# Kernel optimization log

Hardware: AMD Instinct MI355X
Metric: run time of the kernel (lower is better)

Reference implementation:

```python
import jax, jax.numpy as jnp
import numpy as np

B, NQ, NP, C, H = 8, 1024, 2048, 1024, 16
D = C // H  # head_dim = 64


def setup_inputs() -> dict:
    key = jax.random.key(0)
    ks = jax.random.split(key, 12)
    s = 1.0 / np.sqrt(C)
    inp = {
        "x": jax.random.normal(ks[0], (B, NQ, C), dtype=jnp.float32),
        "ctx": jax.random.normal(ks[1], (B, NP, C), dtype=jnp.float32),
        "freqs_cis": jax.random.normal(ks[2], (NP, D // 2, 2), dtype=jnp.float32),
        "wq": jax.random.normal(ks[3], (C, C), dtype=jnp.float32) * s,
        "bq": jnp.zeros((C,), dtype=jnp.float32),
        "wk": jax.random.normal(ks[4], (C, C), dtype=jnp.float32) * s,
        "bk": jnp.zeros((C,), dtype=jnp.float32),
        "wv": jax.random.normal(ks[5], (C, C), dtype=jnp.float32) * s,
        "bv": jnp.zeros((C,), dtype=jnp.float32),
        "wo": jax.random.normal(ks[6], (C, C), dtype=jnp.float32) * s,
        "bo": jnp.zeros((C,), dtype=jnp.float32),
    }
    return inp


def _apply_rope(k, freqs_cis):
    # k: [B, Np, H, D]; freqs_cis: [Np, D//2, 2] (cos, sin)
    b, n, h, d = k.shape
    kp = k.reshape(b, n, h, d // 2, 2)  # adjacent-pair complex convention
    kr, ki = kp[..., 0], kp[..., 1]
    cos = freqs_cis[None, :, None, :, 0]
    sin = freqs_cis[None, :, None, :, 1]
    out_r = kr * cos - ki * sin
    out_i = kr * sin + ki * cos
    return jnp.stack([out_r, out_i], axis=-1).reshape(b, n, h, d)


def reference(x, ctx, freqs_cis, wq, bq, wk, bk, wv, bv, wo, bo):
    b, nq, c = x.shape
    npx = ctx.shape[1]
    q = (jnp.einsum('bsc,oc->bso', x, wq) + bq).reshape(b, nq, H, D)
    k = (jnp.einsum('bsc,oc->bso', ctx, wk) + bk).reshape(b, npx, H, D)
    v = (jnp.einsum('bsc,oc->bso', ctx, wv) + bv).reshape(b, npx, H, D)
    k = _apply_rope(k, freqs_cis)
    scale = 1.0 / jnp.sqrt(jnp.asarray(D, dtype=q.dtype))
    scores = jnp.einsum('bqhd,bkhd->bhqk', q, k) * scale
    attn = jax.nn.softmax(scores, axis=-1)
    out = jnp.einsum('bhqk,bkhd->bqhd', attn, v).reshape(b, nq, c)
    return jnp.einsum('bsc,oc->bso', out, wo) + bo
```

## Files before the change

### kernel.cpp

```cpp
#include <hip/hip_runtime.h>
#include <stdint.h>

typedef __bf16 bf16;
typedef bf16 bf16x8 __attribute__((ext_vector_type(8)));
typedef float f32x4 __attribute__((ext_vector_type(4)));
typedef float f32x16 __attribute__((ext_vector_type(16)));
typedef uint32_t u32x4 __attribute__((ext_vector_type(4)));

static __device__ __forceinline__ void async_cp16(const bf16* gsrc, bf16* ldst) {
  __builtin_amdgcn_global_load_lds(
      (const __attribute__((address_space(1))) uint32_t*)gsrc,
      (__attribute__((address_space(3))) uint32_t*)ldst, 16, 0, 0);
}

static __device__ __forceinline__ f32x16 mfma32(bf16x8 a, bf16x8 b, f32x16 c) {
  return __builtin_amdgcn_mfma_f32_32x32x16_bf16(a, b, c, 0, 0, 0);
}
static __device__ __forceinline__ f32x4 mfma16(bf16x8 a, bf16x8 b, f32x4 c) {
  return __builtin_amdgcn_mfma_f32_16x16x32_bf16(a, b, c, 0, 0, 0);
}

static __device__ __forceinline__ uint32_t cvtpk(float lo, float hi) {
  uint32_t r;
  asm("v_cvt_pk_bf16_f32 %0, %1, %2" : "=v"(r) : "v"(lo), "v"(hi));
  return r;
}
static __device__ __forceinline__ void plswap(uint32_t& a, uint32_t& b) {
  asm("v_permlane32_swap_b32 %0, %1" : "+v"(a), "+v"(b));
}

__global__ __launch_bounds__(256) void convert_all(
    const float* __restrict__ x, const float* __restrict__ ctx,
    const float* __restrict__ wq, const float* __restrict__ wk,
    const float* __restrict__ wv, const float* __restrict__ wo,
    bf16* __restrict__ xb, bf16* __restrict__ cb,
    bf16* __restrict__ wqb, bf16* __restrict__ wkb,
    bf16* __restrict__ wvb, bf16* __restrict__ wob) {
  int id = blockIdx.x;
  const float* s; bf16* d; int base;
  if (id < 8192)        { s = x;   d = xb;  base = id; }
  else if (id < 24576)  { s = ctx; d = cb;  base = id - 8192; }
  else if (id < 25600)  { s = wq;  d = wqb; base = id - 24576; }
  else if (id < 26624)  { s = wk;  d = wkb; base = id - 25600; }
  else if (id < 27648)  { s = wv;  d = wvb; base = id - 26624; }
  else                  { s = wo;  d = wob; base = id - 27648; }
  int i = base * 256 + threadIdx.x;
  float4 v = ((const float4*)s)[i];
  ushort4 o;
  o.x = __builtin_bit_cast(unsigned short, (bf16)v.x);
  o.y = __builtin_bit_cast(unsigned short, (bf16)v.y);
  o.z = __builtin_bit_cast(unsigned short, (bf16)v.z);
  o.w = __builtin_bit_cast(unsigned short, (bf16)v.w);
  ((ushort4*)d)[i] = o;
}

template <int OUT_F32, int BIAS_ROW = 0, int ROPE = 0>
__global__ __launch_bounds__(256) void gemm_bt(
    const bf16* __restrict__ A, const bf16* __restrict__ Bw,
    const float* __restrict__ bias, void* __restrict__ Cout,
    int M, int N, int K, float oscale, const float* __restrict__ freqs) {
  __shared__ __align__(16) bf16 sA[128 * 32];
  __shared__ __align__(16) bf16 sB[128 * 32];

  int per = gridDim.x >> 3;
  int id = blockIdx.x;
  int swz = (id & 7) * per + (id >> 3);
  int NB = N >> 7;
  int mb = swz / NB, nb = swz % NB;

  int t = threadIdx.x;
  int l = t & 63, w = t >> 6;
  int wr = (w >> 1) * 64, wc = (w & 1) * 64;
  int lr = l & 15, lk = (l >> 4) * 8;

  const bf16* Abase = A + (size_t)(mb * 128 + (t >> 2)) * K + (t & 3) * 8;
  const bf16* Bbase = Bw + (size_t)(nb * 128 + (t >> 2)) * K + (t & 3) * 8;
  bf16* ldsA = sA + w * 512;
  bf16* ldsB = sB + w * 512;

  f32x4 acc[4][4];
  for (int i = 0; i < 4; i++)
    for (int j = 0; j < 4; j++) acc[i][j] = f32x4{0.f, 0.f, 0.f, 0.f};

  for (int k0 = 0; k0 < K; k0 += 32) {
    async_cp16(Abase + k0, ldsA);
    async_cp16(Abase + k0 + (size_t)64 * K, ldsA + 2048);
    async_cp16(Bbase + k0, ldsB);
    async_cp16(Bbase + k0 + (size_t)64 * K, ldsB + 2048);
    __syncthreads();
    bf16x8 af[4], bfr[4];
    for (int mf = 0; mf < 4; mf++)
      af[mf] = *(const bf16x8*)&sA[(wr + mf * 16 + lr) * 32 + lk];
    for (int nf = 0; nf < 4; nf++)
      bfr[nf] = *(const bf16x8*)&sB[(wc + nf * 16 + lr) * 32 + lk];
    for (int mf = 0; mf < 4; mf++)
      for (int nf = 0; nf < 4; nf++)
        acc[mf][nf] = mfma16(af[mf], bfr[nf], acc[mf][nf]);
    __syncthreads();
  }

  int row0 = mb * 128 + wr + (l >> 4) * 4;
  int col0 = nb * 128 + wc + lr;
  float sgn = (lr & 1) ? 1.f : -1.f;
  for (int nf = 0; nf < 4; nf++) {
    int c = col0 + nf * 16;
    float bi = BIAS_ROW ? 0.f : bias[c];
    for (int mf = 0; mf < 4; mf++)
      for (int j = 0; j < 4; j++) {
        int r = row0 + mf * 16 + j;
        float v = acc[mf][nf][j] + (BIAS_ROW ? bias[r] : bi);
        if (ROPE) {
          float pv = __shfl_xor(v, 1, 64);
          float2 f = ((const float2*)freqs)[(size_t)(r & 2047) * 32 + ((c & 63) >> 1)];
          v = v * f.x + sgn * pv * f.y;
        }
        v *= oscale;
        if (OUT_F32)
          ((float*)Cout)[(size_t)r * N + c] = v;
        else
          ((bf16*)Cout)[(size_t)r * N + c] = (bf16)v;
      }
  }
}

template <int OUT_F32, int BIAS_ROW, int ROPE>
__global__ __launch_bounds__(512, 2) void gemm256(
    const bf16* __restrict__ A, const bf16* __restrict__ Bw,
    const float* __restrict__ bias, void* __restrict__ Cout,
    int N, int K, float oscale, const float* __restrict__ freqs) {
  __shared__ __align__(16) bf16 sA[2][16384];
  __shared__ __align__(16) bf16 sB[2][16384];

  int per = gridDim.x >> 3;
  int id = blockIdx.x;
  int swz = (id & 7) * per + (id >> 3);
  int NB = N >> 8;
  int mb = swz / NB, nb = swz % NB;

  int tid = threadIdx.x;
  int l = tid & 63, w = tid >> 6;
  int wm = w >> 2, wn = w & 3;
  int lr = l & 15, kg = l >> 4;

  int rw = w * 8 + (l >> 3);
  int cs = ((l & 7) ^ ((l >> 3) & 7)) * 8;
  const bf16* Ab = A + (size_t)(mb * 256 + rw) * K + cs;
  const bf16* Bb = Bw + (size_t)(nb * 256 + rw) * K + cs;

  auto stA = [&](int kt, int half, int buf) {
    const bf16* g = Ab + (size_t)(half * 128) * K + kt * 64;
    bf16* d = &sA[buf][half * 8192 + w * 512];
    async_cp16(g, d);
    async_cp16(g + (size_t)64 * K, d + 4096);
  };
  auto stB = [&](int kt, int half, int buf) {
    const bf16* g = Bb + (size_t)(half * 128) * K + kt * 64;
    bf16* d = &sB[buf][half * 8192 + w * 512];
    async_cp16(g, d);
    async_cp16(g + (size_t)64 * K, d + 4096);
  };

  f32x4 acc[8][4];
#pragma unroll
  for (int i = 0; i < 8; i++)
#pragma unroll
    for (int j = 0; j < 4; j++) acc[i][j] = f32x4{0.f, 0.f, 0.f, 0.f};

  int NT = K >> 6;

  stA(0, 0, 0); stA(0, 1, 0); stB(0, 0, 0); stB(0, 1, 0);
  asm volatile("s_waitcnt vmcnt(0)" ::: "memory");
  __builtin_amdgcn_s_barrier();

  int cur = 0;
  for (int t = 0; t < NT; ++t) {
    bool pf = (t + 1 < NT);
    if (pf) {
      stA(t + 1, 0, cur ^ 1);
      asm volatile("s_waitcnt vmcnt(2)" ::: "memory");
    } else {
      asm volatile("s_waitcnt vmcnt(0)" ::: "memory");
    }
    __builtin_amdgcn_s_barrier();

    const bf16* pA = sA[cur];
    const bf16* pB = sB[cur];
    bf16x8 afr[4][2], bq0[2][2], bq1[2][2];

    auto rdA = [&](int mh, int mf, int ks) {
      int rT = wm * 128 + mh * 64 + mf * 16 + lr;
      return *(const bf16x8*)&pA[rT * 64 + (((ks << 2) | kg) ^ (lr & 7)) * 8];
    };
    auto rdB = [&](int nfg, int ks) {
      int rT = wn * 64 + nfg * 16 + lr;
      return *(const bf16x8*)&pB[rT * 64 + (((ks << 2) | kg) ^ (lr & 7)) * 8];
    };

#pragma unroll
    for (int mf = 0; mf < 4; mf++) { afr[mf][0] = rdA(0, mf, 0); afr[mf][1] = rdA(0, mf, 1); }
#pragma unroll
    for (int nf = 0; nf < 2; nf++) { bq0[nf][0] = rdB(nf, 0); bq0[nf][1] = rdB(nf, 1); }
    __builtin_amdgcn_s_barrier();
    __builtin_amdgcn_s_setprio(1);
#pragma unroll
    for (int mf = 0; mf < 4; mf++)
#pragma unroll
      for (int nf = 0; nf < 2; nf++)
#pragma unroll
        for (int ks = 0; ks < 2; ks++)
          acc[mf][nf] = mfma16(afr[mf][ks], bq0[nf][ks], acc[mf][nf]);
    __builtin_amdgcn_s_setprio(0);
    __builtin_amdgcn_s_barrier();

#pragma unroll
    for (int nf = 0; nf < 2; nf++) { bq1[nf][0] = rdB(2 + nf, 0); bq1[nf][1] = rdB(2 + nf, 1); }
    if (pf) stA(t + 1, 1, cur ^ 1);
    __builtin_amdgcn_s_barrier();
    __builtin_amdgcn_s_setprio(1);
#pragma unroll
    for (int mf = 0; mf < 4; mf++)
#pragma unroll
      for (int nf = 0; nf < 2; nf++)
#pragma unroll
        for (int ks = 0; ks < 2; ks++)
          acc[mf][2 + nf] = mfma16(afr[mf][ks], bq1[nf][ks], acc[mf][2 + nf]);
    __builtin_amdgcn_s_setprio(0);
    __builtin_amdgcn_s_barrier();

#pragma unroll
    for (int mf = 0; mf < 4; mf++) { afr[mf][0] = rdA(1, mf, 0); afr[mf][1] = rdA(1, mf, 1); }
    if (pf) stB(t + 1, 0, cur ^ 1);
    __builtin_amdgcn_s_barrier();
    __builtin_amdgcn_s_setprio(1);
#pragma unroll
    for (int mf = 0; mf < 4; mf++)
#pragma unroll
      for (int nf = 0; nf < 2; nf++)
#pragma unroll
        for (int ks = 0; ks < 2; ks++)
          acc[4 + mf][2 + nf] = mfma16(afr[mf][ks], bq1[nf][ks], acc[4 + mf][2 + nf]);
    __builtin_amdgcn_s_setprio(0);
    __builtin_amdgcn_s_barrier();

    if (pf) stB(t + 1, 1, cur ^ 1);
    __builtin_amdgcn_s_barrier();
    __builtin_amdgcn_s_setprio(1);
#pragma unroll
    for (int mf = 0; mf < 4; mf++)
#pragma unroll
      for (int nf = 0; nf < 2; nf++)
#pragma unroll
        for (int ks = 0; ks < 2; ks++)
          acc[4 + mf][nf] = mfma16(afr[mf][ks], bq0[nf][ks], acc[4 + mf][nf]);
    __builtin_amdgcn_s_setprio(0);
    __builtin_amdgcn_s_barrier();

    cur ^= 1;
  }

  int row0 = mb * 256 + wm * 128 + (l >> 4) * 4;
  int col0 = nb * 256 + wn * 64 + lr;
  float sgn = (lr & 1) ? 1.f : -1.f;
#pragma unroll
  for (int fc = 0; fc < 4; fc++) {
    int c = col0 + fc * 16;
    float bi = BIAS_ROW ? 0.f : bias[c];
#pragma unroll
    for (int fr = 0; fr < 8; fr++) {
#pragma unroll
      for (int j = 0; j < 4; j++) {
        int r = row0 + fr * 16 + j;
        float v = acc[fr][fc][j] + (BIAS_ROW ? bias[r] : bi);
        if (ROPE) {
          float pv = __shfl_xor(v, 1, 64);
          float2 f = ((const float2*)freqs)[(size_t)(r & 2047) * 32 + ((c & 63) >> 1)];
          v = v * f.x + sgn * pv * f.y;
        }
        v *= oscale;
        if (OUT_F32)
          ((float*)Cout)[(size_t)r * N + c] = v;
        else
          ((bf16*)Cout)[(size_t)r * N + c] = (bf16)v;
      }
    }
  }
}

__global__ __launch_bounds__(256, 4) void attn_fwd(
    const bf16* __restrict__ Q, const bf16* __restrict__ Kb,
    const bf16* __restrict__ VT, bf16* __restrict__ O) {
  __shared__ __align__(16) bf16 sK[2][4096];
  __shared__ __align__(16) bf16 sV[2][4096];

  int nblk = blockIdx.x;
  int bh = (nblk & 7) * 16 + (nblk >> 6);
  int qt = (nblk >> 3) & 7;
  int b = bh >> 4, h = bh & 15;

  int t = threadIdx.x, l = t & 63, w = t >> 6;
  int ln = l & 31, hi = l >> 5;

  int qg = qt * 128 + w * 32 + ln;
  const bf16* qp = Q + ((size_t)(b * 1024 + qg) * 16 + h) * 64 + hi * 8;
  bf16x8 qf[4];
#pragma unroll
  for (int ds = 0; ds < 4; ds++) qf[ds] = *(const bf16x8*)(qp + ds * 16);

  const bf16* kbase = Kb + ((size_t)b * 2048 * 16 + h) * 64;
  const bf16* vtbase = VT + (size_t)(h * 64) * 16384 + b * 2048;

  int krow = w * 8 + (l >> 3);
  int cg1 = ((l & 7) ^ (krow & 7) ^ ((krow >> 3) & 7)) * 8;
  int r2 = krow + 32;
  int cg2 = ((l & 7) ^ (r2 & 7) ^ ((r2 >> 3) & 7)) * 8;

  auto stageK = [&](int kv0, int nb) {
    async_cp16(kbase + (size_t)(kv0 + krow) * 1024 + cg1, &sK[nb][w * 512]);
    async_cp16(kbase + (size_t)(kv0 + r2) * 1024 + cg2, &sK[nb][2048 + w * 512]);
  };
  auto stageV = [&](int kv0, int nb) {
    async_cp16(vtbase + (size_t)krow * 16384 + kv0 + cg1, &sV[nb][w * 512]);
    async_cp16(vtbase + (size_t)r2 * 16384 + kv0 + cg2, &sV[nb][2048 + w * 512]);
  };

  f32x16 o0, o1, s0, s1, lacc, zero16;
#pragma unroll
  for (int i = 0; i < 16; i++) {
    o0[i] = 0.f; o1[i] = 0.f; lacc[i] = 0.f; zero16[i] = 0.f;
  }
  uint32_t one2 = 0x3f803f80u;
  u32x4 onesw; onesw[0] = one2; onesw[1] = one2; onesw[2] = one2; onesw[3] = one2;
  bf16x8 onesf = __builtin_bit_cast(bf16x8, onesw);

  stageK(0, 0);
  stageV(0, 0);
  __syncthreads();
  int cur = 0;

  int x0 = ((ln & 7) ^ (ln >> 3)) << 3;
  int x1 = x0 ^ (4 << 3);

  for (int tt = 0; tt < 32; tt++) {
    if (tt < 31) { stageK(tt * 64 + 64, cur ^ 1); stageV(tt * 64 + 64, cur ^ 1); }

    __builtin_amdgcn_s_setprio(1);
    {
      int boff = hi * 8;
      bf16x8 kf0 = *(const bf16x8*)&sK[cur][ln * 64 + (boff ^ x0)];
      bf16x8 kf1 = *(const bf16x8*)&sK[cur][(ln + 32) * 64 + (boff ^ x1)];
      s0 = mfma32(kf0, qf[0], zero16);
      s1 = mfma32(kf1, qf[0], zero16);
    }
#pragma unroll
    for (int ds = 1; ds < 4; ds++) {
      int boff = ds * 16 + hi * 8;
      bf16x8 kf0 = *(const bf16x8*)&sK[cur][ln * 64 + (boff ^ x0)];
      bf16x8 kf1 = *(const bf16x8*)&sK[cur][(ln + 32) * 64 + (boff ^ x1)];
      s0 = mfma32(kf0, qf[ds], s0);
      s1 = mfma32(kf1, qf[ds], s1);
    }
    __builtin_amdgcn_s_setprio(0);

#pragma unroll
    for (int i = 0; i < 16; i++) {
      s0[i] = __builtin_amdgcn_exp2f(s0[i]);
      s1[i] = __builtin_amdgcn_exp2f(s1[i]);
    }

    bf16x8 pa[4];
    auto mkfrags = [&](const f32x16& sv, int base) {
#pragma unroll
      for (int u = 0; u < 2; u++) {
        uint32_t w0a = cvtpk(sv[8 * u + 0], sv[8 * u + 1]);
        uint32_t w0b = cvtpk(sv[8 * u + 4], sv[8 * u + 5]);
        plswap(w0a, w0b);
        uint32_t w1a = cvtpk(sv[8 * u + 2], sv[8 * u + 3]);
        uint32_t w1b = cvtpk(sv[8 * u + 6], sv[8 * u + 7]);
        plswap(w1a, w1b);
        u32x4 tmp;
        tmp[0] = w0a; tmp[1] = w1a; tmp[2] = w0b; tmp[3] = w1b;
        pa[base + u] = __builtin_bit_cast(bf16x8, tmp);
      }
    };
    mkfrags(s0, 0);
    mkfrags(s1, 2);

    __builtin_amdgcn_s_setprio(1);
#pragma unroll
    for (int ks = 0; ks < 4; ks++) {
      int koff = ks * 16 + hi * 8;
      bf16x8 vf0 = *(const bf16x8*)&sV[cur][ln * 64 + (koff ^ x0)];
      bf16x8 vf1 = *(const bf16x8*)&sV[cur][(ln + 32) * 64 + (koff ^ x1)];
      o0 = mfma32(vf0, pa[ks], o0);
      o1 = mfma32(vf1, pa[ks], o1);
      lacc = mfma32(onesf, pa[ks], lacc);
    }
    __builtin_amdgcn_s_setprio(0);

    __syncthreads();
    cur ^= 1;
  }

  float inv = __builtin_amdgcn_rcpf(lacc[0]);
  bf16* obase = O + ((size_t)(b * 1024 + qt * 128 + w * 32 + ln) * 16 + h) * 64;
#pragma unroll
  for (int g = 0; g < 4; g++) {
    ushort4 p0, p1;
    p0.x = __builtin_bit_cast(unsigned short, (bf16)(o0[4 * g + 0] * inv));
    p0.y = __builtin_bit_cast(unsigned short, (bf16)(o0[4 * g + 1] * inv));
    p0.z = __builtin_bit_cast(unsigned short, (bf16)(o0[4 * g + 2] * inv));
    p0.w = __builtin_bit_cast(unsigned short, (bf16)(o0[4 * g + 3] * inv));
    p1.x = __builtin_bit_cast(unsigned short, (bf16)(o1[4 * g + 0] * inv));
    p1.y = __builtin_bit_cast(unsigned short, (bf16)(o1[4 * g + 1] * inv));
    p1.z = __builtin_bit_cast(unsigned short, (bf16)(o1[4 * g + 2] * inv));
    p1.w = __builtin_bit_cast(unsigned short, (bf16)(o1[4 * g + 3] * inv));
    *(ushort4*)&obase[8 * g + 4 * hi] = p0;
    *(ushort4*)&obase[32 + 8 * g + 4 * hi] = p1;
  }
}

extern "C" void kernel_launch(void* const* d_in, const int* in_sizes, int n_in,
                              void* d_out, int out_size, void* d_ws, size_t ws_size,
                              hipStream_t stream) {
  const float* x     = (const float*)d_in[0];
  const float* ctx   = (const float*)d_in[1];
  const float* freqs = (const float*)d_in[2];
  const float* wq    = (const float*)d_in[3];
  const float* bq    = (const float*)d_in[4];
  const float* wk    = (const float*)d_in[5];
  const float* bk    = (const float*)d_in[6];
  const float* wv    = (const float*)d_in[7];
  const float* bv    = (const float*)d_in[8];
  const float* wo    = (const float*)d_in[9];
  const float* bo    = (const float*)d_in[10];

  char* p = (char*)d_ws;
  bf16* xb  = (bf16*)p; p += (size_t)8192 * 1024 * 2;
  bf16* cb  = (bf16*)p; p += (size_t)16384 * 1024 * 2;
  bf16* wqb = (bf16*)p; p += (size_t)1024 * 1024 * 2;
  bf16* wkb = (bf16*)p; p += (size_t)1024 * 1024 * 2;
  bf16* wvb = (bf16*)p; p += (size_t)1024 * 1024 * 2;
  bf16* wob = (bf16*)p; p += (size_t)1024 * 1024 * 2;
  bf16* qb  = (bf16*)p; p += (size_t)8192 * 1024 * 2;
  bf16* kb  = (bf16*)p; p += (size_t)16384 * 1024 * 2;
  bf16* vt  = (bf16*)p; p += (size_t)16384 * 1024 * 2;
  bf16* ob  = xb;

  const float K2 = 0.18033688011112042f;

  convert_all<<<28672, 256, 0, stream>>>(x, ctx, wq, wk, wv, wo,
                                         xb, cb, wqb, wkb, wvb, wob);
  gemm_bt<0><<<512, 256, 0, stream>>>(xb, wqb, bq, qb, 8192, 1024, 1024, K2, nullptr);
  gemm256<0, 0, 1><<<256, 512, 0, stream>>>(cb, wkb, bk, kb, 1024, 1024, 1.0f, freqs);
  gemm256<0, 1, 0><<<256, 512, 0, stream>>>(wvb, cb, bv, vt, 16384, 1024, 1.0f, nullptr);
  attn_fwd<<<1024, 256, 0, stream>>>(qb, kb, vt, ob);
  gemm_bt<1><<<512, 256, 0, stream>>>(ob, wob, bo, d_out, 8192, 1024, 1024, 1.0f, nullptr);
}
```

Before: 277.1 us.

## Merge Q, K and V projection GEMMs into one grouped 256-tile launch

Replaces the separate Q GEMM (gemm_bt) and the two gemm256 launches for K (with RoPE) and transposed V with a single 640-block kernel. Each block selects its problem from its swizzled block index. This removes two launches and their tail effects, lets the three projections share the GPU at once, and moves Q onto the 256x256 tile path. The epilogue now branches at runtime on rope and bias-row flags instead of using template constants, which may cost registers or add divergence-free branching overhead.

```diff
diff --git a/kernel.cpp b/kernel.cpp
--- a/kernel.cpp
+++ b/kernel.cpp
@@ -123,19 +123,31 @@
   }
 }
 
-template <int OUT_F32, int BIAS_ROW, int ROPE>
-__global__ __launch_bounds__(512, 2) void gemm256(
-    const bf16* __restrict__ A, const bf16* __restrict__ Bw,
-    const float* __restrict__ bias, void* __restrict__ Cout,
-    int N, int K, float oscale, const float* __restrict__ freqs) {
+__global__ __launch_bounds__(512, 2) void qkv_mega(
+    const bf16* __restrict__ xb, const bf16* __restrict__ cb,
+    const bf16* __restrict__ wqb, const bf16* __restrict__ wkb,
+    const bf16* __restrict__ wvb,
+    const float* __restrict__ bq, const float* __restrict__ bk,
+    const float* __restrict__ bv,
+    bf16* __restrict__ qb, bf16* __restrict__ kb, bf16* __restrict__ vt,
+    const float* __restrict__ freqs, float qscale) {
   __shared__ __align__(16) bf16 sA[2][16384];
   __shared__ __align__(16) bf16 sB[2][16384];
 
-  int per = gridDim.x >> 3;
+  const int K = 1024, NT = 16;
+
   int id = blockIdx.x;
-  int swz = (id & 7) * per + (id >> 3);
-  int NB = N >> 8;
-  int mb = swz / NB, nb = swz % NB;
+  int swz = (id & 7) * 80 + (id >> 3);
+
+  const bf16 *A, *Bw;
+  const float* bias;
+  bf16* out;
+  int N, NB, sid, rope = 0, brow = 0;
+  float osc = 1.0f;
+  if (swz < 128)      { A = xb;  Bw = wqb; bias = bq; out = qb; N = 1024;  NB = 4;  sid = swz;       osc = qscale; }
+  else if (swz < 384) { A = cb;  Bw = wkb; bias = bk; out = kb; N = 1024;  NB = 4;  sid = swz - 128; rope = 1; }
+  else                { A = wvb; Bw = cb;  bias = bv; out = vt; N = 16384; NB = 64; sid = swz - 384; brow = 1; }
+  int mb = sid / NB, nb = sid % NB;
 
   int tid = threadIdx.x;
   int l = tid & 63, w = tid >> 6;
@@ -166,8 +178,6 @@
 #pragma unroll
     for (int j = 0; j < 4; j++) acc[i][j] = f32x4{0.f, 0.f, 0.f, 0.f};
 
-  int NT = K >> 6;
-
   stA(0, 0, 0); stA(0, 1, 0); stB(0, 0, 0); stB(0, 1, 0);
   asm volatile("s_waitcnt vmcnt(0)" ::: "memory");
   __builtin_amdgcn_s_barrier();
@@ -264,23 +274,20 @@
 #pragma unroll
   for (int fc = 0; fc < 4; fc++) {
     int c = col0 + fc * 16;
-    float bi = BIAS_ROW ? 0.f : bias[c];
+    float bi = brow ? 0.f : bias[c];
 #pragma unroll
     for (int fr = 0; fr < 8; fr++) {
 #pragma unroll
       for (int j = 0; j < 4; j++) {
         int r = row0 + fr * 16 + j;
-        float v = acc[fr][fc][j] + (BIAS_ROW ? bias[r] : bi);
-        if (ROPE) {
+        float v = acc[fr][fc][j] + (brow ? bias[r] : bi);
+        if (rope) {
           float pv = __shfl_xor(v, 1, 64);
           float2 f = ((const float2*)freqs)[(size_t)(r & 2047) * 32 + ((c & 63) >> 1)];
           v = v * f.x + sgn * pv * f.y;
         }
-        v *= oscale;
-        if (OUT_F32)
-          ((float*)Cout)[(size_t)r * N + c] = v;
-        else
-          ((bf16*)Cout)[(size_t)r * N + c] = (bf16)v;
+        v *= osc;
+        out[(size_t)r * N + c] = (bf16)v;
       }
     }
   }
@@ -450,9 +457,8 @@
 
   convert_all<<<28672, 256, 0, stream>>>(x, ctx, wq, wk, wv, wo,
                                          xb, cb, wqb, wkb, wvb, wob);
-  gemm_bt<0><<<512, 256, 0, stream>>>(xb, wqb, bq, qb, 8192, 1024, 1024, K2, nullptr);
-  gemm256<0, 0, 1><<<256, 512, 0, stream>>>(cb, wkb, bk, kb, 1024, 1024, 1.0f, freqs);
-  gemm256<0, 1, 0><<<256, 512, 0, stream>>>(wvb, cb, bv, vt, 16384, 1024, 1.0f, nullptr);
+  qkv_mega<<<640, 512, 0, stream>>>(xb, cb, wqb, wkb, wvb, bq, bk, bv,
+                                    qb, kb, vt, freqs, K2);
   attn_fwd<<<1024, 256, 0, stream>>>(qb, kb, vt, ob);
   gemm_bt<1><<<512, 256, 0, stream>>>(ob, wob, bo, d_out, 8192, 1024, 1024, 1.0f, nullptr);
 }
```

Result: slower. 371.4 us (+34.0%).

## Software-pipeline attention loop with triple-buffered K and overlapped QK/PV

Applied to the files above, without the earlier changes.

Restructures the attention inner loop so the QK^T MFMAs for the next KV tile are issued before the softmax and PV of the current tile. K gets a third LDS buffer so K runs two tiles ahead of V, and the loop is unrolled by two to alternate score registers. The aim is to hide exp and convert latency and LDS loads behind matrix work. The cost is extra LDS (three K buffers), which may reduce occupancy under launch_bounds 4, and more live registers for the second score set.

```diff
diff --git a/kernel.cpp b/kernel.cpp
--- a/kernel.cpp
+++ b/kernel.cpp
@@ -289,7 +289,7 @@
 __global__ __launch_bounds__(256, 4) void attn_fwd(
     const bf16* __restrict__ Q, const bf16* __restrict__ Kb,
     const bf16* __restrict__ VT, bf16* __restrict__ O) {
-  __shared__ __align__(16) bf16 sK[2][4096];
+  __shared__ __align__(16) bf16 sK[3][4096];
   __shared__ __align__(16) bf16 sV[2][4096];
 
   int nblk = blockIdx.x;
@@ -314,16 +314,16 @@
   int r2 = krow + 32;
   int cg2 = ((l & 7) ^ (r2 & 7) ^ ((r2 >> 3) & 7)) * 8;
 
-  auto stageK = [&](int kv0, int nb) {
-    async_cp16(kbase + (size_t)(kv0 + krow) * 1024 + cg1, &sK[nb][w * 512]);
-    async_cp16(kbase + (size_t)(kv0 + r2) * 1024 + cg2, &sK[nb][2048 + w * 512]);
-  };
-  auto stageV = [&](int kv0, int nb) {
-    async_cp16(vtbase + (size_t)krow * 16384 + kv0 + cg1, &sV[nb][w * 512]);
-    async_cp16(vtbase + (size_t)r2 * 16384 + kv0 + cg2, &sV[nb][2048 + w * 512]);
-  };
-
-  f32x16 o0, o1, s0, s1, lacc, zero16;
+  auto stageK = [&](int kv0, int slot) {
+    async_cp16(kbase + (size_t)(kv0 + krow) * 1024 + cg1, &sK[slot][w * 512]);
+    async_cp16(kbase + (size_t)(kv0 + r2) * 1024 + cg2, &sK[slot][2048 + w * 512]);
+  };
+  auto stageV = [&](int kv0, int slot) {
+    async_cp16(vtbase + (size_t)krow * 16384 + kv0 + cg1, &sV[slot][w * 512]);
+    async_cp16(vtbase + (size_t)r2 * 16384 + kv0 + cg2, &sV[slot][2048 + w * 512]);
+  };
+
+  f32x16 o0, o1, lacc, zero16;
 #pragma unroll
   for (int i = 0; i < 16; i++) {
     o0[i] = 0.f; o1[i] = 0.f; lacc[i] = 0.f; zero16[i] = 0.f;
@@ -332,41 +332,34 @@
   u32x4 onesw; onesw[0] = one2; onesw[1] = one2; onesw[2] = one2; onesw[3] = one2;
   bf16x8 onesf = __builtin_bit_cast(bf16x8, onesw);
 
-  stageK(0, 0);
-  stageV(0, 0);
-  __syncthreads();
-  int cur = 0;
-
   int x0 = ((ln & 7) ^ (ln >> 3)) << 3;
   int x1 = x0 ^ (4 << 3);
 
-  for (int tt = 0; tt < 32; tt++) {
-    if (tt < 31) { stageK(tt * 64 + 64, cur ^ 1); stageV(tt * 64 + 64, cur ^ 1); }
-
-    __builtin_amdgcn_s_setprio(1);
+  auto qk = [&](int slot, f32x16& d0, f32x16& d1) {
+    const bf16* pK = sK[slot];
     {
       int boff = hi * 8;
-      bf16x8 kf0 = *(const bf16x8*)&sK[cur][ln * 64 + (boff ^ x0)];
-      bf16x8 kf1 = *(const bf16x8*)&sK[cur][(ln + 32) * 64 + (boff ^ x1)];
-      s0 = mfma32(kf0, qf[0], zero16);
-      s1 = mfma32(kf1, qf[0], zero16);
+      bf16x8 kf0 = *(const bf16x8*)&pK[ln * 64 + (boff ^ x0)];
+      bf16x8 kf1 = *(const bf16x8*)&pK[(ln + 32) * 64 + (boff ^ x1)];
+      d0 = mfma32(kf0, qf[0], zero16);
+      d1 = mfma32(kf1, qf[0], zero16);
     }
 #pragma unroll
     for (int ds = 1; ds < 4; ds++) {
       int boff = ds * 16 + hi * 8;
-      bf16x8 kf0 = *(const bf16x8*)&sK[cur][ln * 64 + (boff ^ x0)];
-      bf16x8 kf1 = *(const bf16x8*)&sK[cur][(ln + 32) * 64 + (boff ^ x1)];
-      s0 = mfma32(kf0, qf[ds], s0);
-      s1 = mfma32(kf1, qf[ds], s1);
-    }
-    __builtin_amdgcn_s_setprio(0);
-
+      bf16x8 kf0 = *(const bf16x8*)&pK[ln * 64 + (boff ^ x0)];
+      bf16x8 kf1 = *(const bf16x8*)&pK[(ln + 32) * 64 + (boff ^ x1)];
+      d0 = mfma32(kf0, qf[ds], d0);
+      d1 = mfma32(kf1, qf[ds], d1);
+    }
+  };
+
+  auto softmax_pv = [&](f32x16& s0, f32x16& s1, int vslot) {
 #pragma unroll
     for (int i = 0; i < 16; i++) {
       s0[i] = __builtin_amdgcn_exp2f(s0[i]);
       s1[i] = __builtin_amdgcn_exp2f(s1[i]);
     }
-
     bf16x8 pa[4];
     auto mkfrags = [&](const f32x16& sv, int base) {
 #pragma unroll
@@ -385,20 +378,47 @@
     mkfrags(s0, 0);
     mkfrags(s1, 2);
 
+    const bf16* pV = sV[vslot];
     __builtin_amdgcn_s_setprio(1);
 #pragma unroll
     for (int ks = 0; ks < 4; ks++) {
       int koff = ks * 16 + hi * 8;
-      bf16x8 vf0 = *(const bf16x8*)&sV[cur][ln * 64 + (koff ^ x0)];
-      bf16x8 vf1 = *(const bf16x8*)&sV[cur][(ln + 32) * 64 + (koff ^ x1)];
+      bf16x8 vf0 = *(const bf16x8*)&pV[ln * 64 + (koff ^ x0)];
+      bf16x8 vf1 = *(const bf16x8*)&pV[(ln + 32) * 64 + (koff ^ x1)];
       o0 = mfma32(vf0, pa[ks], o0);
       o1 = mfma32(vf1, pa[ks], o1);
       lacc = mfma32(onesf, pa[ks], lacc);
     }
     __builtin_amdgcn_s_setprio(0);
-
-    __syncthreads();
-    cur ^= 1;
+  };
+
+  stageK(0, 0);
+  stageK(64, 1);
+  stageV(0, 0);
+  __syncthreads();
+
+  f32x16 sa0, sa1, sb0, sb1;
+  qk(0, sa0, sa1);
+
+  int rs = 1, ws = 2;
+  for (int tt = 0; tt < 32; tt += 2) {
+    {
+      stageV((tt + 1) * 64, (tt + 1) & 1);
+      if (tt < 30) stageK((tt + 2) * 64, ws);
+      qk(rs, sb0, sb1);
+      softmax_pv(sa0, sa1, tt & 1);
+      __syncthreads();
+      int f = 3 - rs - ws; rs = ws; ws = f;
+    }
+    {
+      int t1 = tt + 1;
+      if (t1 < 31) stageV((t1 + 1) * 64, (t1 + 1) & 1);
+      if (t1 < 30) stageK((t1 + 2) * 64, ws);
+      if (t1 < 31) qk(rs, sa0, sa1);
+      softmax_pv(sb0, sb1, t1 & 1);
+      __syncthreads();
+      int f = 3 - rs - ws; rs = ws; ws = f;
+    }
   }
 
   float inv = __builtin_amdgcn_rcpf(lacc[0]);
```

New measurement: 753.4 us. +171.9%, slower.
